# Optimization experiments

Hardware: AMD Instinct MI355X
Metric: run time of the kernel (lower is better)

The kernel has to match this reference:

```python
import jax, jax.numpy as jnp
import numpy as np

B, S, DIN, DOUT = 4, 2048, 4096, 4096

def setup_inputs() -> dict:
    key = jax.random.key(0)
    k1, k2, k3, k4 = jax.random.split(key, 4)
    x = jax.random.normal(k1, (B, S, DIN), dtype=jnp.float32)
    # int8 per-channel quantized weight (stored here as int32 holding int8 range values)
    weight = jax.random.randint(k2, (DOUT, DIN), -127, 128, dtype=jnp.int32)
    weight_scale = jax.random.uniform(k3, (DOUT,), dtype=jnp.float32, minval=0.001, maxval=0.02)
    weight_offset = jax.random.randint(k4, (DOUT,), -8, 8, dtype=jnp.int32)
    return {"x": x, "weight": weight, "weight_scale": weight_scale, "weight_offset": weight_offset}

def reference(x, weight, weight_scale, weight_offset):
    # W8A16 weight-only dequant: per-output-channel (w - offset) * scale, then GEMM.
    w_fp = (weight.astype(x.dtype) - weight_offset.astype(x.dtype)[:, None]) * weight_scale.astype(x.dtype)[:, None]  # [DOUT, DIN]
    # [B,S,DIN] @ [DOUT,DIN]^T -> [B,S,DOUT]
    return jnp.einsum('bsd,od->bso', x, w_fp)
```

## Files before the change

### kernel.cpp

```cpp
#include <hip/hip_runtime.h>
#include <stdint.h>

#define DIN   4096
#define DOUT  4096
#define MTOT  8192
#define NT    64

#define BM    256
#define BN    256
#define GRID_M (MTOT / BM)
#define GRID_N (DOUT / BN)
#define NWG   (GRID_M * GRID_N)

typedef __attribute__((ext_vector_type(4))) float        f32x4;
typedef __attribute__((ext_vector_type(4))) int          i32x4;
typedef __attribute__((ext_vector_type(4))) unsigned int u32x4;
typedef __attribute__((ext_vector_type(2))) unsigned int u32x2;
typedef __attribute__((ext_vector_type(8))) short        bf16x8;

__device__ __forceinline__ unsigned int pack_bf2_rne(float a, float b) {
  unsigned int ua = __builtin_bit_cast(unsigned int, a);
  unsigned int ub = __builtin_bit_cast(unsigned int, b);
  ua += 0x7fffu + ((ua >> 16) & 1u);
  ub += 0x7fffu + ((ub >> 16) & 1u);
  return (ua >> 16) | (ub & 0xffff0000u);
}

__device__ __forceinline__ unsigned int pack_bf2_exact(int a, int b) {
  unsigned int ua = __builtin_bit_cast(unsigned int, (float)a);
  unsigned int ub = __builtin_bit_cast(unsigned int, (float)b);
  return (ua >> 16) | (ub & 0xffff0000u);
}

__global__ __launch_bounds__(256) void convA_kernel(const float* __restrict__ X,
                                                    u32x4* __restrict__ wsA) {
  const int total = MTOT * (DIN / 8);
  for (int idx = blockIdx.x * 256 + threadIdx.x; idx < total; idx += gridDim.x * 256) {
    const int m  = idx >> 9;
    const int c  = idx & 511;
    const int kt = c >> 3, ch = c & 7;
    const int rb = m >> 7, row = m & 127;
    const f32x4* src = (const f32x4*)(X + ((long)m << 12) + kt * 64 + ch * 8);
    f32x4 f0 = src[0], f1 = src[1];
    u32x4 d;
    d[0] = pack_bf2_rne(f0[0], f0[1]);
    d[1] = pack_bf2_rne(f0[2], f0[3]);
    d[2] = pack_bf2_rne(f1[0], f1[1]);
    d[3] = pack_bf2_rne(f1[2], f1[3]);
    wsA[(long)(rb * NT + kt) * 1024 + row * 8 + (ch ^ (row & 7))] = d;
  }
}

__global__ __launch_bounds__(256) void convB_kernel(const int* __restrict__ W,
                                                    const int* __restrict__ Off,
                                                    u32x4* __restrict__ wsB) {
  const int total = DOUT * (DIN / 8);
  for (int idx = blockIdx.x * 256 + threadIdx.x; idx < total; idx += gridDim.x * 256) {
    const int n  = idx >> 9;
    const int c  = idx & 511;
    const int kt = c >> 3, ch = c & 7;
    const int nb = n >> 7, row = n & 127;
    const i32x4* src = (const i32x4*)(W + ((long)n << 12) + kt * 64 + ch * 8);
    const int off = Off[n];
    i32x4 w0 = src[0], w1 = src[1];
    u32x4 d;
    d[0] = pack_bf2_exact(w0[0] - off, w0[1] - off);
    d[1] = pack_bf2_exact(w0[2] - off, w0[3] - off);
    d[2] = pack_bf2_exact(w1[0] - off, w1[1] - off);
    d[3] = pack_bf2_exact(w1[2] - off, w1[3] - off);
    wsB[(long)(nb * NT + kt) * 1024 + row * 8 + (ch ^ (row & 7))] = d;
  }
}


#define BAR()   __builtin_amdgcn_s_barrier()
#define SB()    __builtin_amdgcn_sched_barrier(0)
#define LGKM0() asm volatile("s_waitcnt lgkmcnt(0)" ::: "memory")
#define WAITV(N) asm volatile("s_waitcnt vmcnt(" #N ")" ::: "memory")

typedef __attribute__((address_space(3))) const char* ldsp;

#define DSR(dst, p, IMM) \
  asm volatile("ds_read_b128 %0, %1 offset:" #IMM : "=v"(dst) : "v"(p))

#define STAGE(ldsArr, bufc, h, basePtr, t)                                      \
  { const u32x4* s_ = (basePtr) + (long)(t) * 1024;                             \
    _Pragma("unroll")                                                           \
    for (int i_ = 0; i_ < 2; ++i_) {                                            \
      const int o_ = tid + i_ * 512;                                            \
      __builtin_amdgcn_global_load_lds(                                         \
          (const __attribute__((address_space(1))) void*)(s_ + o_),             \
          (__attribute__((address_space(3))) void*)(&ldsArr[bufc][h][0][0] + o_),\
          16, 0, 0);                                                            \
    } }

#define RD_P1(pAc0, pBc0)                                                       \
  DSR(aP[0], pAc0, 0);    DSR(aP[1], pAc0, 2048);                               \
  DSR(aP[2], pAc0, 4096); DSR(aP[3], pAc0, 6144);                               \
  DSR(bP[0], pBc0, 0);    DSR(bP[1], pBc0, 2048);                               \
  DSR(bP[2], pBc0, 4096); DSR(bP[3], pBc0, 6144);
#define RD_P2(pAc1, pBc1)                                                       \
  DSR(aQ[0], pAc1, 0);    DSR(aQ[1], pAc1, 2048);                               \
  DSR(aQ[2], pAc1, 4096); DSR(aQ[3], pAc1, 6144);                               \
  DSR(bQ[0], pBc1, 0);    DSR(bQ[1], pBc1, 2048);                               \
  DSR(bQ[2], pBc1, 4096); DSR(bQ[3], pBc1, 6144);
#define RD_P3(pAc0)                                                             \
  DSR(aP[0], pAc0, 8192);  DSR(aP[1], pAc0, 10240);                             \
  DSR(aP[2], pAc0, 12288); DSR(aP[3], pAc0, 14336);
#define RD_P4(pAc1)                                                             \
  DSR(aQ[0], pAc1, 8192);  DSR(aQ[1], pAc1, 10240);                             \
  DSR(aQ[2], pAc1, 12288); DSR(aQ[3], pAc1, 14336);

#define MMA16(aS_, bS_, mb)                                                     \
  __builtin_amdgcn_s_setprio(1);                                                \
  { _Pragma("unroll") for (int m_ = 0; m_ < 4; ++m_)                            \
    { _Pragma("unroll") for (int n_ = 0; n_ < 4; ++n_)                          \
        acc[(mb) + m_][n_] = __builtin_amdgcn_mfma_f32_16x16x32_bf16(           \
            aS_[m_], bS_[n_], acc[(mb) + m_][n_], 0, 0, 0); } }                 \
  __builtin_amdgcn_s_setprio(0);

#define TILE(pAc0, pAc1, pBc0, pBc1, ABUF, BBUF, t, SA, SBf, WV)                \
  RD_P1(pAc0, pBc0)                                                             \
  if (SA) { STAGE(ldsA, ABUF, 0, bA0, (t) + 1) }                                \
  BAR(); LGKM0(); SB(); MMA16(aP, bP, 0) BAR();                                 \
  RD_P2(pAc1, pBc1)                                                             \
  if (SA) { STAGE(ldsA, ABUF, 1, bA1, (t) + 1) }                                \
  BAR(); LGKM0(); SB(); MMA16(aQ, bQ, 0) BAR();                                 \
  RD_P3(pAc0)                                                                   \
  if (SBf) { STAGE(ldsB, BBUF, 0, bB0, (t) + 2) }                               \
  BAR(); LGKM0(); SB(); MMA16(aP, bP, 4) BAR();                                 \
  RD_P4(pAc1)                                                                   \
  if (SBf) { STAGE(ldsB, BBUF, 1, bB1, (t) + 2) }                               \
  WV; BAR(); LGKM0(); SB(); MMA16(aQ, bQ, 4) BAR();

__global__ __launch_bounds__(512, 2) void gemm8_kernel(
    const u32x4* __restrict__ wsA, const u32x4* __restrict__ wsB,
    const float* __restrict__ Scale, float* __restrict__ Out) {
  __shared__ u32x4 ldsA[2][2][128][8];
  __shared__ u32x4 ldsB[2][2][128][8];

  const int tid  = threadIdx.x;
  const int lane = tid & 63;
  const int wid  = tid >> 6;
  const int wr   = wid >> 2;
  const int wc   = wid & 3;
  const int wch  = wc >> 1;
  const int wcl  = wc & 1;

  int gid = (int)blockIdx.x;
  gid = (gid & 7) * (NWG >> 3) + (gid >> 3);
  const int wg_m = gid / GRID_N;
  const int wg_n = gid % GRID_N;

  const int riA = lane & 15;
  const int c0  = lane >> 4;
  const int cs0 = c0 ^ (riA & 7);
  const int cs1 = (4 + c0) ^ (riA & 7);

  ldsp pA0c0 = (ldsp)&ldsA[0][wr][riA][cs0];
  ldsp pA0c1 = (ldsp)&ldsA[0][wr][riA][cs1];
  ldsp pA1c0 = (ldsp)&ldsA[1][wr][riA][cs0];
  ldsp pA1c1 = (ldsp)&ldsA[1][wr][riA][cs1];
  ldsp pB0c0 = (ldsp)&ldsB[0][wch][wcl * 64 + riA][cs0];
  ldsp pB0c1 = (ldsp)&ldsB[0][wch][wcl * 64 + riA][cs1];
  ldsp pB1c0 = (ldsp)&ldsB[1][wch][wcl * 64 + riA][cs0];
  ldsp pB1c1 = (ldsp)&ldsB[1][wch][wcl * 64 + riA][cs1];

  const u32x4* bA0 = wsA + (long)(wg_m * 2 + 0) * NT * 1024;
  const u32x4* bA1 = wsA + (long)(wg_m * 2 + 1) * NT * 1024;
  const u32x4* bB0 = wsB + (long)(wg_n * 2 + 0) * NT * 1024;
  const u32x4* bB1 = wsB + (long)(wg_n * 2 + 1) * NT * 1024;

  f32x4 acc[8][4];
#pragma unroll
  for (int m = 0; m < 8; ++m)
#pragma unroll
    for (int n = 0; n < 4; ++n) acc[m][n] = (f32x4){0.f, 0.f, 0.f, 0.f};

  bf16x8 aP[4], aQ[4], bP[4], bQ[4];

  STAGE(ldsB, 0, 0, bB0, 0) STAGE(ldsA, 0, 0, bA0, 0)
  STAGE(ldsB, 0, 1, bB1, 0) STAGE(ldsA, 0, 1, bA1, 0)
  STAGE(ldsB, 1, 0, bB0, 1) STAGE(ldsB, 1, 1, bB1, 1)
  WAITV(4); BAR();

#pragma unroll 1
  for (int it = 0; it < 31; ++it) {
    const int t = 2 * it;
    TILE(pA0c0, pA0c1, pB0c0, pB0c1, 1, 0, t,     1, 1, WAITV(4))
    TILE(pA1c0, pA1c1, pB1c0, pB1c1, 0, 1, t + 1, 1, 1, WAITV(4))
  }
  TILE(pA0c0, pA0c1, pB0c0, pB0c1, 1, 0, 62, 1, 0, WAITV(0))
  TILE(pA1c0, pA1c1, pB1c0, pB1c1, 0, 1, 63, 0, 0, )

  const int col0 = wg_n * BN + wc * 64 + (lane & 15);
  const int row0 = wg_m * BM + wr * 128 + ((lane >> 4) << 2);
#pragma unroll
  for (int n = 0; n < 4; ++n) {
    const int col = col0 + n * 16;
    const float s = Scale[col];
#pragma unroll
    for (int m = 0; m < 8; ++m) {
      const int r = row0 + m * 16;
#pragma unroll
      for (int j = 0; j < 4; ++j)
        Out[(long)(r + j) * DOUT + col] = acc[m][n][j] * s;
    }
  }
}

__global__ __launch_bounds__(256, 2) void gemm_fused_kernel(
    const float* __restrict__ X, const int* __restrict__ W,
    const int* __restrict__ Off, const float* __restrict__ Scale,
    float* __restrict__ Out) {
  __shared__ char ldsA[2][128 * 64 * 2];
  __shared__ char ldsB[2][128 * 64 * 2];

  const int tid  = threadIdx.x;
  const int lane = tid & 63;
  const int wid  = tid >> 6;
  const int fwr  = wid >> 1;
  const int fwc  = wid & 1;

  int gid = (int)blockIdx.x;
  gid = (gid & 7) * (2048 >> 3) + (gid >> 3);
  const int wg_m = gid / 32;
  const int wg_n = gid % 32;
  const int brow = wg_m * 128;
  const int bcol = wg_n * 128;

  f32x4 acc[4][4];
#pragma unroll
  for (int m = 0; m < 4; ++m)
#pragma unroll
    for (int n = 0; n < 4; ++n) acc[m][n] = (f32x4){0.f, 0.f, 0.f, 0.f};

  int aoff[2][4], boff[2][4];
#pragma unroll
  for (int kk = 0; kk < 2; ++kk)
#pragma unroll
    for (int m = 0; m < 4; ++m) {
      const int kb = kk * 64 + ((lane >> 4) << 4);
      const int ra = fwr * 64 + m * 16 + (lane & 15);
      const int rb = fwc * 64 + m * 16 + (lane & 15);
      aoff[kk][m] = ra * 128 + (kb ^ ((ra & 7) << 4));
      boff[kk][m] = rb * 128 + (kb ^ ((rb & 7) << 4));
    }

  long xo[8], wo[8];
  int lo[8], ofv[8];
#pragma unroll
  for (int i = 0; i < 8; ++i) {
    const int idx = tid + i * 256;
    const int row = idx >> 4, c4 = idx & 15;
    xo[i] = (long)(brow + row) * DIN + c4 * 4;
    wo[i] = (long)(bcol + row) * DIN + c4 * 4;
    lo[i] = row * 128 + ((c4 * 8) ^ ((row & 7) << 4));
    ofv[i] = Off[bcol + row];
  }
  {
#pragma unroll
    for (int i = 0; i < 8; ++i) {
      f32x4 f = *(const f32x4*)(X + xo[i]);
      u32x2 d;
      d[0] = pack_bf2_rne(f[0], f[1]);
      d[1] = pack_bf2_rne(f[2], f[3]);
      *(u32x2*)(&ldsA[0][lo[i]]) = d;
    }
#pragma unroll
    for (int i = 0; i < 8; ++i) {
      i32x4 w = *(const i32x4*)(W + wo[i]);
      u32x2 d;
      d[0] = pack_bf2_exact(w[0] - ofv[i], w[1] - ofv[i]);
      d[1] = pack_bf2_exact(w[2] - ofv[i], w[3] - ofv[i]);
      *(u32x2*)(&ldsB[0][lo[i]]) = d;
    }
  }
  __syncthreads();
#pragma unroll 1
  for (int kt = 0; kt < NT; ++kt) {
    const int cur = kt & 1;
    const bool pf = (kt + 1 < NT);
    f32x4 fa[8];
    i32x4 fb[8];
    if (pf) {
      const int ko = (kt + 1) * 64;
#pragma unroll
      for (int i = 0; i < 8; ++i) fa[i] = *(const f32x4*)(X + xo[i] + ko);
#pragma unroll
      for (int i = 0; i < 8; ++i) fb[i] = *(const i32x4*)(W + wo[i] + ko);
    }
#pragma unroll
    for (int kk = 0; kk < 2; ++kk) {
      bf16x8 fa2[4], fb2[4];
#pragma unroll
      for (int m = 0; m < 4; ++m)
        fa2[m] = __builtin_bit_cast(bf16x8, *(const u32x4*)(&ldsA[cur][aoff[kk][m]]));
#pragma unroll
      for (int n = 0; n < 4; ++n)
        fb2[n] = __builtin_bit_cast(bf16x8, *(const u32x4*)(&ldsB[cur][boff[kk][n]]));
#pragma unroll
      for (int m = 0; m < 4; ++m)
#pragma unroll
        for (int n = 0; n < 4; ++n)
          acc[m][n] = __builtin_amdgcn_mfma_f32_16x16x32_bf16(fa2[m], fb2[n], acc[m][n], 0, 0, 0);
    }
    if (pf) {
      char* dA = ldsA[cur ^ 1];
      char* dB = ldsB[cur ^ 1];
#pragma unroll
      for (int i = 0; i < 8; ++i) {
        u32x2 d;
        d[0] = pack_bf2_rne(fa[i][0], fa[i][1]);
        d[1] = pack_bf2_rne(fa[i][2], fa[i][3]);
        *(u32x2*)(&dA[lo[i]]) = d;
      }
#pragma unroll
      for (int i = 0; i < 8; ++i) {
        u32x2 d;
        d[0] = pack_bf2_exact(fb[i][0] - ofv[i], fb[i][1] - ofv[i]);
        d[1] = pack_bf2_exact(fb[i][2] - ofv[i], fb[i][3] - ofv[i]);
        *(u32x2*)(&dB[lo[i]]) = d;
      }
    }
    __syncthreads();
  }

  const int col0 = bcol + fwc * 64 + (lane & 15);
  const int row0 = brow + fwr * 64 + ((lane >> 4) << 2);
#pragma unroll
  for (int n = 0; n < 4; ++n) {
    const int col = col0 + n * 16;
    const float s = Scale[col];
#pragma unroll
    for (int m = 0; m < 4; ++m) {
      const int r = row0 + m * 16;
#pragma unroll
      for (int j = 0; j < 4; ++j)
        Out[(long)(r + j) * DOUT + col] = acc[m][n][j] * s;
    }
  }
}

extern "C" void kernel_launch(void* const* d_in, const int* in_sizes, int n_in,
                              void* d_out, int out_size, void* d_ws, size_t ws_size,
                              hipStream_t stream) {
  (void)in_sizes; (void)n_in; (void)out_size;
  const float* X  = (const float*)d_in[0];
  const int*   W  = (const int*)d_in[1];
  const float* Sc = (const float*)d_in[2];
  const int*   Of = (const int*)d_in[3];
  float* Out = (float*)d_out;

  const size_t needA = (size_t)MTOT * DIN * 2;
  const size_t needB = (size_t)DOUT * DIN * 2;
  if (ws_size >= needA + needB) {
    u32x4* wsA = (u32x4*)d_ws;
    u32x4* wsB = (u32x4*)((char*)d_ws + needA);
    convA_kernel<<<2048, 256, 0, stream>>>(X, wsA);
    convB_kernel<<<2048, 256, 0, stream>>>(W, Of, wsB);
    gemm8_kernel<<<NWG, 512, 0, stream>>>(wsA, wsB, Sc, Out);
  } else {
    gemm_fused_kernel<<<2048, 256, 0, stream>>>(X, W, Of, Sc, Out);
  }
}
```

Measured before the change: 275.3 us.

## Software-pipeline LDS fragment reads one phase ahead of MFMA

Reorders the per-tile LDS read phases so each phase reads the fragments needed by the next MFMA block, with the first phase of the next tile prefetched during the last phase of the current one. Partial lgkmcnt waits replace full drains, so ds_reads overlap MFMA work instead of stalling before each block. The vmcnt wait for the next B tile is moved earlier, to before the third phase. This adds register-lifetime pressure and makes correctness depend on precise wait counts and buffer hazards across barriers.

```diff
diff --git a/kernel.cpp b/kernel.cpp
--- a/kernel.cpp
+++ b/kernel.cpp
@@ -75,7 +75,8 @@
 
 #define BAR()   __builtin_amdgcn_s_barrier()
 #define SB()    __builtin_amdgcn_sched_barrier(0)
-#define LGKM0() asm volatile("s_waitcnt lgkmcnt(0)" ::: "memory")
+#define LGKM_(N) asm volatile("s_waitcnt lgkmcnt(" #N ")" ::: "memory")
+#define LGKM(N)  LGKM_(N)
 #define WAITV(N) asm volatile("s_waitcnt vmcnt(" #N ")" ::: "memory")
 
 typedef __attribute__((address_space(3))) const char* ldsp;
@@ -94,22 +95,22 @@
           16, 0, 0);                                                            \
     } }
 
-#define RD_P1(pAc0, pBc0)                                                       \
+#define RD_QLO(pAc1, pBc1)                                                      \
+  DSR(aQ[0], pAc1, 0);    DSR(aQ[1], pAc1, 2048);                               \
+  DSR(aQ[2], pAc1, 4096); DSR(aQ[3], pAc1, 6144);                               \
+  DSR(bQ[0], pBc1, 0);    DSR(bQ[1], pBc1, 2048);                               \
+  DSR(bQ[2], pBc1, 4096); DSR(bQ[3], pBc1, 6144);
+#define RD_PHI(pAc0)                                                            \
+  DSR(aP[0], pAc0, 8192);  DSR(aP[1], pAc0, 10240);                             \
+  DSR(aP[2], pAc0, 12288); DSR(aP[3], pAc0, 14336);
+#define RD_QHI(pAc1)                                                            \
+  DSR(aQ[0], pAc1, 8192);  DSR(aQ[1], pAc1, 10240);                             \
+  DSR(aQ[2], pAc1, 12288); DSR(aQ[3], pAc1, 14336);
+#define RD_PLO(pAc0, pBc0)                                                      \
   DSR(aP[0], pAc0, 0);    DSR(aP[1], pAc0, 2048);                               \
   DSR(aP[2], pAc0, 4096); DSR(aP[3], pAc0, 6144);                               \
   DSR(bP[0], pBc0, 0);    DSR(bP[1], pBc0, 2048);                               \
   DSR(bP[2], pBc0, 4096); DSR(bP[3], pBc0, 6144);
-#define RD_P2(pAc1, pBc1)                                                       \
-  DSR(aQ[0], pAc1, 0);    DSR(aQ[1], pAc1, 2048);                               \
-  DSR(aQ[2], pAc1, 4096); DSR(aQ[3], pAc1, 6144);                               \
-  DSR(bQ[0], pBc1, 0);    DSR(bQ[1], pBc1, 2048);                               \
-  DSR(bQ[2], pBc1, 4096); DSR(bQ[3], pBc1, 6144);
-#define RD_P3(pAc0)                                                             \
-  DSR(aP[0], pAc0, 8192);  DSR(aP[1], pAc0, 10240);                             \
-  DSR(aP[2], pAc0, 12288); DSR(aP[3], pAc0, 14336);
-#define RD_P4(pAc1)                                                             \
-  DSR(aQ[0], pAc1, 8192);  DSR(aQ[1], pAc1, 10240);                             \
-  DSR(aQ[2], pAc1, 12288); DSR(aQ[3], pAc1, 14336);
 
 #define MMA16(aS_, bS_, mb)                                                     \
   __builtin_amdgcn_s_setprio(1);                                                \
@@ -119,19 +120,19 @@
             aS_[m_], bS_[n_], acc[(mb) + m_][n_], 0, 0, 0); } }                 \
   __builtin_amdgcn_s_setprio(0);
 
-#define TILE(pAc0, pAc1, pBc0, pBc1, ABUF, BBUF, t, SA, SBf, WV)                \
-  RD_P1(pAc0, pBc0)                                                             \
+#define TILE(pAc0, pAc1, pBc0, pBc1, pAc0N, pBc0N, ABUF, BBUF, t, SA, SBf, WV3, RDN, L4) \
+  RD_QLO(pAc1, pBc1)                                                            \
   if (SA) { STAGE(ldsA, ABUF, 0, bA0, (t) + 1) }                                \
-  BAR(); LGKM0(); SB(); MMA16(aP, bP, 0) BAR();                                 \
-  RD_P2(pAc1, pBc1)                                                             \
+  BAR(); LGKM(8); SB(); MMA16(aP, bP, 0) BAR();                                 \
+  RD_PHI(pAc0)                                                                  \
   if (SA) { STAGE(ldsA, ABUF, 1, bA1, (t) + 1) }                                \
-  BAR(); LGKM0(); SB(); MMA16(aQ, bQ, 0) BAR();                                 \
-  RD_P3(pAc0)                                                                   \
+  BAR(); LGKM(4); SB(); MMA16(aQ, bQ, 0) BAR();                                 \
+  RD_QHI(pAc1)                                                                  \
   if (SBf) { STAGE(ldsB, BBUF, 0, bB0, (t) + 2) }                               \
-  BAR(); LGKM0(); SB(); MMA16(aP, bP, 4) BAR();                                 \
-  RD_P4(pAc1)                                                                   \
+  WV3; BAR(); LGKM(4); SB(); MMA16(aP, bP, 4) BAR();                            \
+  if (RDN) { RD_PLO(pAc0N, pBc0N) }                                             \
   if (SBf) { STAGE(ldsB, BBUF, 1, bB1, (t) + 2) }                               \
-  WV; BAR(); LGKM0(); SB(); MMA16(aQ, bQ, 4) BAR();
+  BAR(); LGKM(L4); SB(); MMA16(aQ, bQ, 4) BAR();
 
 __global__ __launch_bounds__(512, 2) void gemm8_kernel(
     const u32x4* __restrict__ wsA, const u32x4* __restrict__ wsB,
@@ -183,15 +184,16 @@
   STAGE(ldsB, 0, 1, bB1, 0) STAGE(ldsA, 0, 1, bA1, 0)
   STAGE(ldsB, 1, 0, bB0, 1) STAGE(ldsB, 1, 1, bB1, 1)
   WAITV(4); BAR();
+  RD_PLO(pA0c0, pB0c0)
 
 #pragma unroll 1
   for (int it = 0; it < 31; ++it) {
     const int t = 2 * it;
-    TILE(pA0c0, pA0c1, pB0c0, pB0c1, 1, 0, t,     1, 1, WAITV(4))
-    TILE(pA1c0, pA1c1, pB1c0, pB1c1, 0, 1, t + 1, 1, 1, WAITV(4))
-  }
-  TILE(pA0c0, pA0c1, pB0c0, pB0c1, 1, 0, 62, 1, 0, WAITV(0))
-  TILE(pA1c0, pA1c1, pB1c0, pB1c1, 0, 1, 63, 0, 0, )
+    TILE(pA0c0, pA0c1, pB0c0, pB0c1, pA1c0, pB1c0, 1, 0, t,     1, 1, WAITV(2), 1, 8)
+    TILE(pA1c0, pA1c1, pB1c0, pB1c1, pA0c0, pB0c0, 0, 1, t + 1, 1, 1, WAITV(2), 1, 8)
+  }
+  TILE(pA0c0, pA0c1, pB0c0, pB0c1, pA1c0, pB1c0, 1, 0, 62, 1, 0, WAITV(0), 1, 8)
+  TILE(pA1c0, pA1c1, pB1c0, pB1c1, pA0c0, pB0c0, 0, 1, 63, 0, 0,          , 0, 0)
 
   const int col0 = wg_n * BN + wc * 64 + (lane & 15);
   const int row0 = wg_m * BM + wr * 128 + ((lane >> 4) << 2);
```

Result: slower. 291.0 us (+5.7%).
